# Kernel optimization log

Measured on AMD Instinct MI355X. Metric: run time of the kernel, lower is better.

## Reference

```python
import jax, jax.numpy as jnp
import numpy as np

B, C, HID, H, W = 32, 1024, 512, 56, 56

def setup_inputs() -> dict:
    key = jax.random.key(0)
    ks = jax.random.split(key, 8)
    s = 0.02
    return {
        "x":  jax.random.normal(ks[0], (B, C, H, W), dtype=jnp.float32),
        "W1": jax.random.normal(ks[1], (C, HID), dtype=jnp.float32) * s,  # mlp Linear(C->hidden), no bias
        "W2": jax.random.normal(ks[2], (HID, C), dtype=jnp.float32) * s,  # mlp Linear(hidden->C), no bias
        "WA": jax.random.normal(ks[3], (C, H), dtype=jnp.float32) * s,    # fc_A weight (transposed)
        "bA": jax.random.normal(ks[4], (H,), dtype=jnp.float32) * s,
        "WB": jax.random.normal(ks[5], (C, W), dtype=jnp.float32) * s,    # fc_B weight (transposed)
        "bB": jax.random.normal(ks[6], (W,), dtype=jnp.float32) * s,
    }

def reference(x, W1, W2, WA, bA, WB, bB):
    # Global average pool over spatial dims: (B, C)
    y = jnp.mean(x, axis=(2, 3))
    # MLP with exact (erf) GELU; dropout is identity in eval mode
    h = jax.nn.gelu(y @ W1, approximate=False)          # (B, HID)
    yp = jax.nn.gelu(h @ W2, approximate=False)          # (B, C)
    # Original replicates yp across C channels before fc_A/fc_B, so every
    # channel's attention map is identical: compute once, broadcast.
    A = yp @ WA + bA                                     # (B, H)
    Bv = yp @ WB + bB                                    # (B, W)
    attn = jax.nn.sigmoid(A[:, None, :, None] * Bv[:, None, None, :])  # (B, 1, H, W)
    return jnp.broadcast_to(attn, (x.shape[0], x.shape[1], A.shape[1], Bv.shape[1]))
```

## Files before the change

kernel.cpp:

```cpp
#include <hip/hip_runtime.h>
#include <math.h>

#define BATCH 32
#define NC    1024
#define NHID  512
#define NH    56
#define NW    56
#define HWSZ  3136
#define HW4   784

typedef float nfloat4 __attribute__((ext_vector_type(4)));

__device__ __forceinline__ float gelu_exact(float x) {
    return 0.5f * x * (1.0f + erff(x * 0.7071067811865476f));
}

__global__ __launch_bounds__(256) void gap_kernel(const float* __restrict__ x,
                                                  float* __restrict__ y,
                                                  const float* __restrict__ W1,
                                                  const float* __restrict__ W2,
                                                  const float* __restrict__ WA,
                                                  const float* __restrict__ WB) {
    const int row  = (blockIdx.x << 2) | (threadIdx.x >> 6);
    const int lane = threadIdx.x & 63;
    const nfloat4* xr = (const nfloat4*)(x + (size_t)row * HWSZ);

    float s = 0.f;
#pragma unroll
    for (int it = 0; it < 12; ++it) {
        nfloat4 v = __builtin_nontemporal_load(xr + lane + (it << 6));
        s += (v.x + v.y) + (v.z + v.w);
    }
    if (lane < 16) {
        nfloat4 v = __builtin_nontemporal_load(xr + 768 + lane);
        s += (v.x + v.y) + (v.z + v.w);
    }
#pragma unroll
    for (int off = 32; off > 0; off >>= 1) s += __shfl_down(s, off);
    if (lane == 0) y[row] = s * (1.0f / 3136.0f);

    const int pb = (int)blockIdx.x - (BATCH * NC / 4 - 1152);
    if (pb >= 0) {
        const int t = threadIdx.x;
        float sink = 0.f;
        if (pb < 512) {
            nfloat4 w = ((const nfloat4*)W1)[pb * 256 + t];
            sink = w.x + w.w;
        } else if (pb < 1024) {
            nfloat4 w = ((const nfloat4*)W2)[(pb - 512) * 256 + t];
            sink = w.x + w.w;
        } else {
            const int q = pb - 1024;
            if (q < 56) {
                nfloat4 w = ((const nfloat4*)WA)[q * 256 + t];
                sink = w.x;
            } else if (q < 112) {
                nfloat4 w = ((const nfloat4*)WB)[(q - 56) * 256 + t];
                sink = w.x;
            }
        }
        asm volatile("" :: "v"(sink));
    }
}

__global__ __launch_bounds__(256) void fc1_kernel(const float* __restrict__ y,
                                                  const float* __restrict__ W1,
                                                  float* __restrict__ h) {
    const int jc = blockIdx.x;
    const int b  = blockIdx.y;
    const int t  = threadIdx.x;

    __shared__ float   sy[NC];
    __shared__ nfloat4 part[256];
    __shared__ nfloat4 spart[64];
    for (int i = t; i < NC; i += 256) sy[i] = y[b * NC + i];
    __syncthreads();

    const int lane8 = t & 7;
    const int j0 = jc * 32 + lane8 * 4;
    const int ks = (t >> 3) * 32;

    nfloat4 acc0 = {0.f, 0.f, 0.f, 0.f};
    nfloat4 acc1 = {0.f, 0.f, 0.f, 0.f};
    const float* wbase = W1 + (size_t)ks * NHID + j0;
#pragma unroll 8
    for (int c = 0; c < 32; c += 2) {
        nfloat4 w0 = *(const nfloat4*)(wbase + (size_t)(c + 0) * NHID);
        nfloat4 w1 = *(const nfloat4*)(wbase + (size_t)(c + 1) * NHID);
        acc0 += sy[ks + c + 0] * w0;
        acc1 += sy[ks + c + 1] * w1;
    }
    part[t] = acc0 + acc1;
    __syncthreads();
    if (t < 64) spart[t] = part[t] + part[t + 64] + part[t + 128] + part[t + 192];
    __syncthreads();
    if (t < 8) {
        nfloat4 s = spart[t];
#pragma unroll
        for (int g = 1; g < 8; ++g) s += spart[g * 8 + t];
        float* hp = h + b * NHID + jc * 32 + t * 4;
        hp[0] = gelu_exact(s.x);
        hp[1] = gelu_exact(s.y);
        hp[2] = gelu_exact(s.z);
        hp[3] = gelu_exact(s.w);
    }
}

__global__ __launch_bounds__(256) void fc2_kernel(const float* __restrict__ h,
                                                  const float* __restrict__ W2,
                                                  float* __restrict__ yp) {
    const int cc = blockIdx.x;
    const int b  = blockIdx.y;
    const int t  = threadIdx.x;

    __shared__ float   sh[NHID];
    __shared__ nfloat4 part[256];
    __shared__ nfloat4 spart[64];
    for (int i = t; i < NHID; i += 256) sh[i] = h[b * NHID + i];
    __syncthreads();

    const int lane8 = t & 7;
    const int c0 = cc * 32 + lane8 * 4;
    const int js = (t >> 3) * 16;

    nfloat4 acc0 = {0.f, 0.f, 0.f, 0.f};
    nfloat4 acc1 = {0.f, 0.f, 0.f, 0.f};
    const float* wbase = W2 + (size_t)js * NC + c0;
#pragma unroll 8
    for (int jj = 0; jj < 16; jj += 2) {
        nfloat4 w0 = *(const nfloat4*)(wbase + (size_t)(jj + 0) * NC);
        nfloat4 w1 = *(const nfloat4*)(wbase + (size_t)(jj + 1) * NC);
        acc0 += sh[js + jj + 0] * w0;
        acc1 += sh[js + jj + 1] * w1;
    }
    part[t] = acc0 + acc1;
    __syncthreads();
    if (t < 64) spart[t] = part[t] + part[t + 64] + part[t + 128] + part[t + 192];
    __syncthreads();
    if (t < 8) {
        nfloat4 s = spart[t];
#pragma unroll
        for (int g = 1; g < 8; ++g) s += spart[g * 8 + t];
        float* pp = yp + b * NC + cc * 32 + t * 4;
        pp[0] = gelu_exact(s.x);
        pp[1] = gelu_exact(s.y);
        pp[2] = gelu_exact(s.z);
        pp[3] = gelu_exact(s.w);
    }
}

__global__ __launch_bounds__(512) void ab_kernel(
    const float* __restrict__ yp, const float* __restrict__ WA,
    const float* __restrict__ bA, const float* __restrict__ WB,
    const float* __restrict__ bB, float* __restrict__ AB) {
    const int b = blockIdx.x;
    const int t = threadIdx.x;

    __shared__ float   sp[NC];
    __shared__ nfloat4 partA[512];
    __shared__ nfloat4 partB[512];
    for (int i = t; i < NC; i += 512) sp[i] = yp[b * NC + i];
    __syncthreads();

    const int grp    = t >> 4;
    const int lane16 = t & 15;
    const int ks     = grp * 32;
    nfloat4 accA = {0.f, 0.f, 0.f, 0.f};
    nfloat4 accB = {0.f, 0.f, 0.f, 0.f};
    if (lane16 < 14) {
        const nfloat4* wa = (const nfloat4*)WA + (size_t)ks * 14 + lane16;
        const nfloat4* wb = (const nfloat4*)WB + (size_t)ks * 14 + lane16;
#pragma unroll 8
        for (int c = 0; c < 32; ++c) {
            const float sv = sp[ks + c];
            accA += sv * wa[(size_t)c * 14];
            accB += sv * wb[(size_t)c * 14];
        }
    }
    partA[t] = accA;
    partB[t] = accB;
    __syncthreads();
    if (t < 16) {
        nfloat4 s = partA[t];
#pragma unroll
        for (int g = 1; g < 32; ++g) s += partA[g * 16 + t];
        if (t < 14) {
            const int i0 = t * 4;
            AB[b * 128 + i0 + 0] = bA[i0 + 0] + s.x;
            AB[b * 128 + i0 + 1] = bA[i0 + 1] + s.y;
            AB[b * 128 + i0 + 2] = bA[i0 + 2] + s.z;
            AB[b * 128 + i0 + 3] = bA[i0 + 3] + s.w;
        }
    } else if (t < 32) {
        const int l = t - 16;
        nfloat4 s = partB[l];
#pragma unroll
        for (int g = 1; g < 32; ++g) s += partB[g * 16 + l];
        if (l < 14) {
            const int i0 = l * 4;
            AB[b * 128 + 64 + i0 + 0] = bB[i0 + 0] + s.x;
            AB[b * 128 + 64 + i0 + 1] = bB[i0 + 1] + s.y;
            AB[b * 128 + 64 + i0 + 2] = bB[i0 + 2] + s.z;
            AB[b * 128 + 64 + i0 + 3] = bB[i0 + 3] + s.w;
        }
    }
}

__global__ __launch_bounds__(256) void bcast_kernel(const float* __restrict__ AB,
                                                    float* __restrict__ out) {
    const int blk = blockIdx.x;
    const int b = blk >> 6;
    const int cchunk = blk & 63;
    const int t = threadIdx.x;

    __shared__ float sA[NH];
    __shared__ float sB[NW];
    if (t < NH) sA[t] = AB[b * 128 + t];
    else if (t >= 64 && t < 64 + NW) sB[t - 64] = AB[b * 128 + t];
    __syncthreads();

    nfloat4 v[4];
#pragma unroll
    for (int it = 0; it < 4; ++it) {
        const int idx = t + it * 256;
        if (idx < HW4) {
            const int r  = idx / 14;
            const int cb = (idx - r * 14) * 4;
            const float a = sA[r];
            nfloat4 q;
            q.x = 1.0f / (1.0f + expf(-(a * sB[cb + 0])));
            q.y = 1.0f / (1.0f + expf(-(a * sB[cb + 1])));
            q.z = 1.0f / (1.0f + expf(-(a * sB[cb + 2])));
            q.w = 1.0f / (1.0f + expf(-(a * sB[cb + 3])));
            v[it] = q;
        }
    }

    const size_t base = ((size_t)b * NC + (size_t)cchunk * 16) * HW4;
#pragma unroll
    for (int ch = 0; ch < 16; ++ch) {
        nfloat4* orow = (nfloat4*)out + base + (size_t)ch * HW4;
#pragma unroll
        for (int it = 0; it < 4; ++it) {
            const int idx = t + it * 256;
            if (idx < HW4) __builtin_nontemporal_store(v[it], &orow[idx]);
        }
    }
}

extern "C" void kernel_launch(void* const* d_in, const int* in_sizes, int n_in,
                              void* d_out, int out_size, void* d_ws, size_t ws_size,
                              hipStream_t stream) {
    const float* x  = (const float*)d_in[0];
    const float* W1 = (const float*)d_in[1];
    const float* W2 = (const float*)d_in[2];
    const float* WA = (const float*)d_in[3];
    const float* bA = (const float*)d_in[4];
    const float* WB = (const float*)d_in[5];
    const float* bB = (const float*)d_in[6];
    float* out = (float*)d_out;

    float* y  = (float*)d_ws;
    float* yp = y;
    float* h  = y + BATCH * NC;
    float* AB = h + BATCH * NHID;

    gap_kernel<<<BATCH * NC / 4, 256, 0, stream>>>(x, y, W1, W2, WA, WB);
    fc1_kernel<<<dim3(NHID / 32, BATCH), 256, 0, stream>>>(y, W1, h);
    fc2_kernel<<<dim3(NC / 32, BATCH), 256, 0, stream>>>(h, W2, yp);
    ab_kernel<<<BATCH, 512, 0, stream>>>(yp, WA, bA, WB, bB, AB);
    bcast_kernel<<<BATCH * (NC / 16), 256, 0, stream>>>(AB, out);
}
```

Baseline: 163.6 us.

## Drop weight prefetch from GAP kernel and stream broadcast map through LDS per wave

Removes the trailing blocks in the pooling kernel that touched W1/W2/WA/WB to warm the cache for later kernels. The broadcast kernel now builds the sigmoid map once in shared memory, padded with a 64-element wrap, and each wave streams four consecutive channels as one contiguous run of 49 full 64-lane stores. This replaces the partial-wave tail stores of the per-channel loop. It adds an LDS buffer and an extra barrier, and it gives up the L2 prefetch of the weights.

```diff
diff --git a/kernel.cpp b/kernel.cpp
--- a/kernel.cpp
+++ b/kernel.cpp
@@ -16,11 +16,7 @@
 }
 
 __global__ __launch_bounds__(256) void gap_kernel(const float* __restrict__ x,
-                                                  float* __restrict__ y,
-                                                  const float* __restrict__ W1,
-                                                  const float* __restrict__ W2,
-                                                  const float* __restrict__ WA,
-                                                  const float* __restrict__ WB) {
+                                                  float* __restrict__ y) {
     const int row  = (blockIdx.x << 2) | (threadIdx.x >> 6);
     const int lane = threadIdx.x & 63;
     const nfloat4* xr = (const nfloat4*)(x + (size_t)row * HWSZ);
@@ -38,29 +34,6 @@
 #pragma unroll
     for (int off = 32; off > 0; off >>= 1) s += __shfl_down(s, off);
     if (lane == 0) y[row] = s * (1.0f / 3136.0f);
-
-    const int pb = (int)blockIdx.x - (BATCH * NC / 4 - 1152);
-    if (pb >= 0) {
-        const int t = threadIdx.x;
-        float sink = 0.f;
-        if (pb < 512) {
-            nfloat4 w = ((const nfloat4*)W1)[pb * 256 + t];
-            sink = w.x + w.w;
-        } else if (pb < 1024) {
-            nfloat4 w = ((const nfloat4*)W2)[(pb - 512) * 256 + t];
-            sink = w.x + w.w;
-        } else {
-            const int q = pb - 1024;
-            if (q < 56) {
-                nfloat4 w = ((const nfloat4*)WA)[q * 256 + t];
-                sink = w.x;
-            } else if (q < 112) {
-                nfloat4 w = ((const nfloat4*)WB)[(q - 56) * 256 + t];
-                sink = w.x;
-            }
-        }
-        asm volatile("" :: "v"(sink));
-    }
 }
 
 __global__ __launch_bounds__(256) void fc1_kernel(const float* __restrict__ y,
@@ -215,36 +188,35 @@
 
     __shared__ float sA[NH];
     __shared__ float sB[NW];
+    __shared__ nfloat4 smap[HW4 + 64];
     if (t < NH) sA[t] = AB[b * 128 + t];
     else if (t >= 64 && t < 64 + NW) sB[t - 64] = AB[b * 128 + t];
     __syncthreads();
 
-    nfloat4 v[4];
-#pragma unroll
-    for (int it = 0; it < 4; ++it) {
-        const int idx = t + it * 256;
-        if (idx < HW4) {
-            const int r  = idx / 14;
-            const int cb = (idx - r * 14) * 4;
-            const float a = sA[r];
-            nfloat4 q;
-            q.x = 1.0f / (1.0f + expf(-(a * sB[cb + 0])));
-            q.y = 1.0f / (1.0f + expf(-(a * sB[cb + 1])));
-            q.z = 1.0f / (1.0f + expf(-(a * sB[cb + 2])));
-            q.w = 1.0f / (1.0f + expf(-(a * sB[cb + 3])));
-            v[it] = q;
-        }
-    }
-
-    const size_t base = ((size_t)b * NC + (size_t)cchunk * 16) * HW4;
-#pragma unroll
-    for (int ch = 0; ch < 16; ++ch) {
-        nfloat4* orow = (nfloat4*)out + base + (size_t)ch * HW4;
-#pragma unroll
-        for (int it = 0; it < 4; ++it) {
-            const int idx = t + it * 256;
-            if (idx < HW4) __builtin_nontemporal_store(v[it], &orow[idx]);
-        }
+    for (int idx = t; idx < HW4 + 64; idx += 256) {
+        const int p  = (idx >= HW4) ? idx - HW4 : idx;
+        const int r  = p / 14;
+        const int cb = (p - r * 14) * 4;
+        const float a = sA[r];
+        nfloat4 q;
+        q.x = 1.0f / (1.0f + expf(-(a * sB[cb + 0])));
+        q.y = 1.0f / (1.0f + expf(-(a * sB[cb + 1])));
+        q.z = 1.0f / (1.0f + expf(-(a * sB[cb + 2])));
+        q.w = 1.0f / (1.0f + expf(-(a * sB[cb + 3])));
+        smap[idx] = q;
+    }
+    __syncthreads();
+
+    const int w    = t >> 6;
+    const int lane = t & 63;
+    nfloat4* op = (nfloat4*)out +
+                  ((size_t)b * NC + (size_t)cchunk * 16 + (size_t)w * 4) * HW4;
+    int pos = 0;
+#pragma unroll 7
+    for (int it = 0; it < 49; ++it) {
+        __builtin_nontemporal_store(smap[pos + lane], &op[it * 64 + lane]);
+        pos += 64;
+        if (pos >= HW4) pos -= HW4;
     }
 }
 
@@ -265,7 +237,7 @@
     float* h  = y + BATCH * NC;
     float* AB = h + BATCH * NHID;
 
-    gap_kernel<<<BATCH * NC / 4, 256, 0, stream>>>(x, y, W1, W2, WA, WB);
+    gap_kernel<<<BATCH * NC / 4, 256, 0, stream>>>(x, y);
     fc1_kernel<<<dim3(NHID / 32, BATCH), 256, 0, stream>>>(y, W1, h);
     fc2_kernel<<<dim3(NC / 32, BATCH), 256, 0, stream>>>(h, W2, yp);
     ab_kernel<<<BATCH, 512, 0, stream>>>(yp, WA, bA, WB, bB, AB);
```

New measurement: 162.1 us. Within noise of the previous version (-0.9%).
